# Optimization experiments

Measured on AMD Instinct MI355X. Metric: run time of the kernel, lower is better.

## Reference

```python
import jax, jax.numpy as jnp
import numpy as np

D_MODEL = 512
SCALE = 1.0 / (D_MODEL ** 0.5)  # module scales by 1/sqrt(d_model), not d_head
NEG = -1000000000.0

def setup_inputs() -> dict:
    key = jax.random.key(0)
    kq, kk, kv, kl = jax.random.split(key, 4)
    B, H, S, Dh = 4, 8, 2048, 64
    Q = jax.random.normal(kq, (B, H, S, Dh), dtype=jnp.float32)
    K = jax.random.normal(kk, (B, H, S, Dh), dtype=jnp.float32)
    V = jax.random.normal(kv, (B, H, S, Dh), dtype=jnp.float32)
    src_batch_lens = jax.random.randint(kl, (B,), 1, S + 1, dtype=jnp.int32)
    return {"Q": Q, "K": K, "V": V, "src_batch_lens": src_batch_lens}

def reference(Q, K, V, src_batch_lens):
    # scores: [B, H, Sq, Sk]
    scores = jnp.einsum('bhqd,bhkd->bhqk', Q, K) * SCALE
    Sk = K.shape[2]
    # mask keys at positions >= per-batch length
    key_mask = jnp.arange(Sk)[None, None, None, :] >= src_batch_lens[:, None, None, None]
    scores = jnp.where(key_mask, NEG, scores)
    attn = jax.nn.softmax(scores, axis=-1)
    # dropout is identity in eval/reference (p=0)
    context = jnp.einsum('bhqk,bhkd->bhqd', attn, V)
    return context
```

## Files before the change

kernel.cpp:

```cpp
#include <hip/hip_runtime.h>


#define S_LEN 2048
#define DH 64
#define QK_SCALE ((float)(1.4426950408889634 / 22.627416997969522))
#define NEG_BIG -1.0e30f

typedef __attribute__((ext_vector_type(8))) short bf16x8;
typedef __attribute__((ext_vector_type(4))) float f32x4;

__device__ __forceinline__ short f2bf(float f) {
    __bf16 h = (__bf16)f;
    return __builtin_bit_cast(short, h);
}

#define SW(r, e) ((e) ^ (((r) & 7) << 3))

__global__ __launch_bounds__(256, 2)
void attn_fwd(const float* __restrict__ Qg, const float* __restrict__ Kg,
              const float* __restrict__ Vg, const int* __restrict__ lens,
              float* __restrict__ Og)
{
    __shared__ short Klds[2][64][64];
    __shared__ short Vt[2][64][64];
    __shared__ short Plds[4][16][64];

    const int tid  = threadIdx.x;
    const int wave = tid >> 6;
    const int lane = tid & 63;
    const int lr   = lane & 15;
    const int lg   = lane >> 4;

    const int bh = blockIdx.y;
    const int L  = lens[bh >> 3];
    const int q0 = blockIdx.x * 64 + wave * 16;
    const size_t base = (size_t)bh * S_LEN * DH;

    bf16x8 qf[2];
    {
        const float* qrow = Qg + base + (size_t)(q0 + lr) * DH + 8 * lg;
        #pragma unroll
        for (int ks = 0; ks < 2; ++ks) {
            float4 a = *(const float4*)(qrow + 32 * ks);
            float4 b = *(const float4*)(qrow + 32 * ks + 4);
            bf16x8 f;
            f[0] = f2bf(a.x * QK_SCALE); f[1] = f2bf(a.y * QK_SCALE);
            f[2] = f2bf(a.z * QK_SCALE); f[3] = f2bf(a.w * QK_SCALE);
            f[4] = f2bf(b.x * QK_SCALE); f[5] = f2bf(b.y * QK_SCALE);
            f[6] = f2bf(b.z * QK_SCALE); f[7] = f2bf(b.w * QK_SCALE);
            qf[ks] = f;
        }
    }

    f32x4 Of[4];
    #pragma unroll
    for (int n = 0; n < 4; ++n) Of[n] = (f32x4){0.f, 0.f, 0.f, 0.f};
    f32x4 Dsum = (f32x4){0.f, 0.f, 0.f, 0.f};
    bf16x8 ones;
    #pragma unroll
    for (int j = 0; j < 8; ++j) ones[j] = (short)0x3F80;

    const int ntiles = (L + 63) >> 6;
    const int krow = tid >> 4;
    const int kc4  = tid & 15;

    float4 kreg[4];
    float  vreg[16];

    {
        const float4* kt = (const float4*)(Kg + base);
        #pragma unroll
        for (int it = 0; it < 4; ++it) kreg[it] = kt[(krow + 16 * it) * 16 + kc4];
        const float* vt = Vg + base;
        #pragma unroll
        for (int i = 0; i < 16; ++i) {
            int key = wave * 16 + ((i + (lane >> 3)) & 15);
            vreg[i] = vt[key * DH + lane];
        }
    }
    {
        #pragma unroll
        for (int it = 0; it < 4; ++it) {
            int row = krow + 16 * it;
            short4 s;
            s.x = f2bf(kreg[it].x); s.y = f2bf(kreg[it].y);
            s.z = f2bf(kreg[it].z); s.w = f2bf(kreg[it].w);
            *(short4*)&Klds[0][row][SW(row, kc4 * 4)] = s;
        }
        #pragma unroll
        for (int i = 0; i < 16; ++i) {
            int key = wave * 16 + ((i + (lane >> 3)) & 15);
            Vt[0][lane][SW(lane, key)] = f2bf(vreg[i]);
        }
    }
    __syncthreads();

    for (int t = 0; t < ntiles; ++t) {
        const int cur = t & 1;
        const bool pre = (t + 1 < ntiles);

        if (pre) {
            const float4* kt = (const float4*)(Kg + base + (size_t)(t + 1) * 64 * DH);
            #pragma unroll
            for (int it = 0; it < 4; ++it) kreg[it] = kt[(krow + 16 * it) * 16 + kc4];
            const float* vt = Vg + base + (size_t)(t + 1) * 64 * DH;
            #pragma unroll
            for (int i = 0; i < 16; ++i) {
                int key = wave * 16 + ((i + (lane >> 3)) & 15);
                vreg[i] = vt[key * DH + lane];
            }
        }

        f32x4 Sv[4];
        #pragma unroll
        for (int n = 0; n < 4; ++n) Sv[n] = (f32x4){0.f, 0.f, 0.f, 0.f};
        #pragma unroll
        for (int ks = 0; ks < 2; ++ks) {
            #pragma unroll
            for (int n = 0; n < 4; ++n) {
                bf16x8 kf = *(const bf16x8*)&Klds[cur][16 * n + lr][SW(16 * n + lr, 8 * lg + 32 * ks)];
                Sv[n] = __builtin_amdgcn_mfma_f32_16x16x32_bf16(qf[ks], kf, Sv[n], 0, 0, 0);
            }
        }

        const int kb = t * 64;
        if (kb + 64 > L) {
            #pragma unroll
            for (int n = 0; n < 4; ++n)
                if (kb + 16 * n + lr >= L) {
                    Sv[n][0] = NEG_BIG; Sv[n][1] = NEG_BIG;
                    Sv[n][2] = NEG_BIG; Sv[n][3] = NEG_BIG;
                }
        }

        #pragma unroll
        for (int r = 0; r < 4; ++r) {
            int q = 4 * lg + r;
            #pragma unroll
            for (int n = 0; n < 4; ++n)
                Plds[wave][q][SW(q, 16 * n + lr)] = f2bf(exp2f(Sv[n][r]));
        }

        #pragma unroll
        for (int ks = 0; ks < 2; ++ks) {
            bf16x8 pf = *(const bf16x8*)&Plds[wave][lr][SW(lr, 8 * lg + 32 * ks)];
            Dsum = __builtin_amdgcn_mfma_f32_16x16x32_bf16(pf, ones, Dsum, 0, 0, 0);
            #pragma unroll
            for (int n = 0; n < 4; ++n) {
                bf16x8 vf = *(const bf16x8*)&Vt[cur][16 * n + lr][SW(16 * n + lr, 8 * lg + 32 * ks)];
                Of[n] = __builtin_amdgcn_mfma_f32_16x16x32_bf16(pf, vf, Of[n], 0, 0, 0);
            }
        }

        if (pre) {
            const int b = cur ^ 1;
            #pragma unroll
            for (int it = 0; it < 4; ++it) {
                int row = krow + 16 * it;
                short4 s;
                s.x = f2bf(kreg[it].x); s.y = f2bf(kreg[it].y);
                s.z = f2bf(kreg[it].z); s.w = f2bf(kreg[it].w);
                *(short4*)&Klds[b][row][SW(row, kc4 * 4)] = s;
            }
            #pragma unroll
            for (int i = 0; i < 16; ++i) {
                int key = wave * 16 + ((i + (lane >> 3)) & 15);
                Vt[b][lane][SW(lane, key)] = f2bf(vreg[i]);
            }
        }
        __syncthreads();
    }

    float inv[4];
    #pragma unroll
    for (int r = 0; r < 4; ++r) inv[r] = 1.f / Dsum[r];
    float* orow = Og + base + (size_t)q0 * DH;
    #pragma unroll
    for (int r = 0; r < 4; ++r) {
        int q = 4 * lg + r;
        #pragma unroll
        for (int n = 0; n < 4; ++n)
            orow[(size_t)q * DH + 16 * n + lr] = Of[n][r] * inv[r];
    }
}

extern "C" void kernel_launch(void* const* d_in, const int* in_sizes, int n_in,
                              void* d_out, int out_size, void* d_ws, size_t ws_size,
                              hipStream_t stream) {
    const float* Q = (const float*)d_in[0];
    const float* K = (const float*)d_in[1];
    const float* V = (const float*)d_in[2];
    const int* lens = (const int*)d_in[3];
    float* O = (float*)d_out;
    dim3 grid(S_LEN / 64, 4 * 8);
    attn_fwd<<<grid, 256, 0, stream>>>(Q, K, V, lens, O);
}
```

Baseline: 136.7 us.

## Split key dimension across blocks with workspace partials and a reduce kernel

Adds a grid z-dimension that splits each head's key range into NS chunks. Blocks whose chunk starts past the batch length exit early. Each remaining block writes unnormalised fp16 partial outputs and fp32 denominators to workspace, and a second kernel sums the partials and normalises. It also interleaves the blockIdx.y to batch/head mapping so that short and long batches are mixed across the grid. The aim is to fix load imbalance from varying sequence lengths and make more blocks available, at the cost of extra workspace traffic, a second launch and fp16 rounding of the partial sums.

```diff
diff --git a/kernel.cpp b/kernel.cpp
--- a/kernel.cpp
+++ b/kernel.cpp
@@ -4,7 +4,6 @@
 #define S_LEN 2048
 #define DH 64
 #define QK_SCALE ((float)(1.4426950408889634 / 22.627416997969522))
-#define NEG_BIG -1.0e30f
 
 typedef __attribute__((ext_vector_type(8))) short bf16x8;
 typedef __attribute__((ext_vector_type(4))) float f32x4;
@@ -13,13 +12,21 @@
     __bf16 h = (__bf16)f;
     return __builtin_bit_cast(short, h);
 }
+__device__ __forceinline__ short f2h(float f) {
+    _Float16 h = (_Float16)f;
+    return __builtin_bit_cast(short, h);
+}
+__device__ __forceinline__ float h2f(short s) {
+    return (float)__builtin_bit_cast(_Float16, s);
+}
 
 #define SW(r, e) ((e) ^ (((r) & 7) << 3))
 
 __global__ __launch_bounds__(256, 2)
 void attn_fwd(const float* __restrict__ Qg, const float* __restrict__ Kg,
               const float* __restrict__ Vg, const int* __restrict__ lens,
-              float* __restrict__ Og)
+              float* __restrict__ Og, short* __restrict__ pW,
+              float* __restrict__ dW, int NS, int CH)
 {
     __shared__ short Klds[2][64][64];
     __shared__ short Vt[2][64][64];
@@ -31,8 +38,13 @@
     const int lr   = lane & 15;
     const int lg   = lane >> 4;
 
-    const int bh = blockIdx.y;
+    const int bh = ((blockIdx.y & 3) << 3) | (blockIdx.y >> 2);
     const int L  = lens[bh >> 3];
+    const int start = blockIdx.z * CH;
+    if (start >= L) return;
+    const int end = min(start + CH, L);
+    const int ntiles = (end - start + 63) >> 6;
+
     const int q0 = blockIdx.x * 64 + wave * 16;
     const size_t base = (size_t)bh * S_LEN * DH;
 
@@ -60,7 +72,6 @@
     #pragma unroll
     for (int j = 0; j < 8; ++j) ones[j] = (short)0x3F80;
 
-    const int ntiles = (L + 63) >> 6;
     const int krow = tid >> 4;
     const int kc4  = tid & 15;
 
@@ -68,10 +79,10 @@
     float  vreg[16];
 
     {
-        const float4* kt = (const float4*)(Kg + base);
+        const float4* kt = (const float4*)(Kg + base + (size_t)start * DH);
         #pragma unroll
         for (int it = 0; it < 4; ++it) kreg[it] = kt[(krow + 16 * it) * 16 + kc4];
-        const float* vt = Vg + base;
+        const float* vt = Vg + base + (size_t)start * DH;
         #pragma unroll
         for (int i = 0; i < 16; ++i) {
             int key = wave * 16 + ((i + (lane >> 3)) & 15);
@@ -97,13 +108,14 @@
 
     for (int t = 0; t < ntiles; ++t) {
         const int cur = t & 1;
+        const int kb = start + t * 64;
         const bool pre = (t + 1 < ntiles);
 
         if (pre) {
-            const float4* kt = (const float4*)(Kg + base + (size_t)(t + 1) * 64 * DH);
+            const float4* kt = (const float4*)(Kg + base + (size_t)(kb + 64) * DH);
             #pragma unroll
             for (int it = 0; it < 4; ++it) kreg[it] = kt[(krow + 16 * it) * 16 + kc4];
-            const float* vt = Vg + base + (size_t)(t + 1) * 64 * DH;
+            const float* vt = Vg + base + (size_t)(kb + 64) * DH;
             #pragma unroll
             for (int i = 0; i < 16; ++i) {
                 int key = wave * 16 + ((i + (lane >> 3)) & 15);
@@ -123,13 +135,12 @@
             }
         }
 
-        const int kb = t * 64;
         if (kb + 64 > L) {
             #pragma unroll
             for (int n = 0; n < 4; ++n)
                 if (kb + 16 * n + lr >= L) {
-                    Sv[n][0] = NEG_BIG; Sv[n][1] = NEG_BIG;
-                    Sv[n][2] = NEG_BIG; Sv[n][3] = NEG_BIG;
+                    Sv[n][0] = -1e30f; Sv[n][1] = -1e30f;
+                    Sv[n][2] = -1e30f; Sv[n][3] = -1e30f;
                 }
         }
 
@@ -171,17 +182,56 @@
         __syncthreads();
     }
 
-    float inv[4];
-    #pragma unroll
-    for (int r = 0; r < 4; ++r) inv[r] = 1.f / Dsum[r];
-    float* orow = Og + base + (size_t)q0 * DH;
-    #pragma unroll
-    for (int r = 0; r < 4; ++r) {
-        int q = 4 * lg + r;
-        #pragma unroll
-        for (int n = 0; n < 4; ++n)
-            orow[(size_t)q * DH + 16 * n + lr] = Of[n][r] * inv[r];
-    }
+    if (NS == 1) {
+        float inv[4];
+        #pragma unroll
+        for (int r = 0; r < 4; ++r) inv[r] = 1.f / Dsum[r];
+        float* orow = Og + base + (size_t)q0 * DH;
+        #pragma unroll
+        for (int r = 0; r < 4; ++r) {
+            int q = 4 * lg + r;
+            #pragma unroll
+            for (int n = 0; n < 4; ++n)
+                orow[(size_t)q * DH + 16 * n + lr] = Of[n][r] * inv[r];
+        }
+    } else {
+        short* prow = pW + ((size_t)(blockIdx.z * 32 + bh) * S_LEN + q0) * DH;
+        #pragma unroll
+        for (int r = 0; r < 4; ++r) {
+            int q = 4 * lg + r;
+            #pragma unroll
+            for (int n = 0; n < 4; ++n)
+                prow[(size_t)q * DH + 16 * n + lr] = f2h(Of[n][r]);
+        }
+        if (lr == 0) {
+            #pragma unroll
+            for (int r = 0; r < 4; ++r)
+                dW[(size_t)(blockIdx.z * 32 + bh) * S_LEN + q0 + 4 * lg + r] = Dsum[r];
+        }
+    }
+}
+
+__global__ __launch_bounds__(256)
+void attn_reduce(const int* __restrict__ lens, const short* __restrict__ pW,
+                 const float* __restrict__ dW, float* __restrict__ Og,
+                 int NS, int CH)
+{
+    const size_t i = ((size_t)blockIdx.x * 256 + threadIdx.x) * 4;
+    const int bh = (int)(i >> 17);
+    const int q  = (int)((i >> 6) & (S_LEN - 1));
+    const int L  = lens[bh >> 3];
+    const int nact = min(NS, (L + CH - 1) / CH);
+
+    float ax = 0.f, ay = 0.f, az = 0.f, aw = 0.f, den = 0.f;
+    for (int s = 0; s < nact; ++s) {
+        const size_t sb = (size_t)(s * 32 + bh);
+        short4 h = *(const short4*)(pW + sb * (S_LEN * DH) + (i & (S_LEN * DH - 1)));
+        ax += h2f(h.x); ay += h2f(h.y); az += h2f(h.z); aw += h2f(h.w);
+        den += dW[sb * S_LEN + q];
+    }
+    const float inv = 1.f / den;
+    float4 o; o.x = ax * inv; o.y = ay * inv; o.z = az * inv; o.w = aw * inv;
+    *(float4*)(Og + i) = o;
 }
 
 extern "C" void kernel_launch(void* const* d_in, const int* in_sizes, int n_in,
@@ -192,6 +242,20 @@
     const float* V = (const float*)d_in[2];
     const int* lens = (const int*)d_in[3];
     float* O = (float*)d_out;
-    dim3 grid(S_LEN / 64, 4 * 8);
-    attn_fwd<<<grid, 256, 0, stream>>>(Q, K, V, lens, O);
-}
+
+    const size_t outN = (size_t)4 * 8 * S_LEN * DH;
+    auto need = [&](int ns) {
+        return (size_t)ns * (outN * 2 + (size_t)32 * S_LEN * 4);
+    };
+    int NS = (ws_size >= need(4)) ? 4 : (ws_size >= need(2)) ? 2 : 1;
+    const int CH = S_LEN / NS;
+
+    short* pW = (short*)d_ws;
+    float* dW = (float*)((char*)d_ws + (size_t)NS * outN * 2);
+
+    dim3 grid1(S_LEN / 64, 4 * 8, NS);
+    attn_fwd<<<grid1, 256, 0, stream>>>(Q, K, V, lens, O, pW, dW, NS, CH);
+    if (NS > 1) {
+        attn_reduce<<<(unsigned)(outN / 1024), 256, 0, stream>>>(lens, pW, dW, O, NS, CH);
+    }
+}
```

Result: slower. 147.7 us (+8.1%).

## Vectorize LDS stores for K, V and P tiles, and interleave batch-head block order

Applied to the files above, without the earlier changes.

K tiles are now staged as 8-wide bf16 LDS stores per thread. Each thread writes V transposed as two 16-byte vectors instead of 16 scalar shorts. The QK MFMA operands are swapped so each lane holds 4 consecutive keys of one query row, which lets P be written to LDS as short4 vectors and changes the mask indexing to match. The blockIdx.y to batch-head mapping is permuted so that neighbouring blocks come from different batches, which spreads the variable sequence lengths across the GPU. The aim is fewer LDS write instructions and less bank traffic, plus better load balance; the new V store pattern may bring bank conflicts and changes the global load coalescing for V.

```diff
diff --git a/kernel.cpp b/kernel.cpp
--- a/kernel.cpp
+++ b/kernel.cpp
@@ -4,7 +4,6 @@
 #define S_LEN 2048
 #define DH 64
 #define QK_SCALE ((float)(1.4426950408889634 / 22.627416997969522))
-#define NEG_BIG -1.0e30f
 
 typedef __attribute__((ext_vector_type(8))) short bf16x8;
 typedef __attribute__((ext_vector_type(4))) float f32x4;
@@ -31,7 +30,7 @@
     const int lr   = lane & 15;
     const int lg   = lane >> 4;
 
-    const int bh = blockIdx.y;
+    const int bh = ((blockIdx.y & 3) << 3) | (blockIdx.y >> 2);
     const int L  = lens[bh >> 3];
     const int q0 = blockIdx.x * 64 + wave * 16;
     const size_t base = (size_t)bh * S_LEN * DH;
@@ -61,54 +60,60 @@
     for (int j = 0; j < 8; ++j) ones[j] = (short)0x3F80;
 
     const int ntiles = (L + 63) >> 6;
-    const int krow = tid >> 4;
-    const int kc4  = tid & 15;
+
+    const int krow = tid >> 3;
+    const int kc8  = (tid & 7) * 8;
 
     float4 kreg[4];
     float  vreg[16];
 
     {
-        const float4* kt = (const float4*)(Kg + base);
-        #pragma unroll
-        for (int it = 0; it < 4; ++it) kreg[it] = kt[(krow + 16 * it) * 16 + kc4];
+        const float* kt = Kg + base;
+        #pragma unroll
+        for (int p = 0; p < 2; ++p) {
+            kreg[2 * p]     = *(const float4*)(kt + (krow + 32 * p) * DH + kc8);
+            kreg[2 * p + 1] = *(const float4*)(kt + (krow + 32 * p) * DH + kc8 + 4);
+        }
         const float* vt = Vg + base;
         #pragma unroll
-        for (int i = 0; i < 16; ++i) {
-            int key = wave * 16 + ((i + (lane >> 3)) & 15);
-            vreg[i] = vt[key * DH + lane];
-        }
+        for (int i = 0; i < 16; ++i)
+            vreg[i] = vt[(wave * 16 + i) * DH + lane];
     }
     {
         #pragma unroll
-        for (int it = 0; it < 4; ++it) {
-            int row = krow + 16 * it;
-            short4 s;
-            s.x = f2bf(kreg[it].x); s.y = f2bf(kreg[it].y);
-            s.z = f2bf(kreg[it].z); s.w = f2bf(kreg[it].w);
-            *(short4*)&Klds[0][row][SW(row, kc4 * 4)] = s;
-        }
-        #pragma unroll
-        for (int i = 0; i < 16; ++i) {
-            int key = wave * 16 + ((i + (lane >> 3)) & 15);
-            Vt[0][lane][SW(lane, key)] = f2bf(vreg[i]);
-        }
+        for (int p = 0; p < 2; ++p) {
+            int row = krow + 32 * p;
+            bf16x8 s;
+            s[0] = f2bf(kreg[2*p].x); s[1] = f2bf(kreg[2*p].y);
+            s[2] = f2bf(kreg[2*p].z); s[3] = f2bf(kreg[2*p].w);
+            s[4] = f2bf(kreg[2*p+1].x); s[5] = f2bf(kreg[2*p+1].y);
+            s[6] = f2bf(kreg[2*p+1].z); s[7] = f2bf(kreg[2*p+1].w);
+            *(bf16x8*)&Klds[0][row][SW(row, kc8)] = s;
+        }
+        bf16x8 a, b;
+        #pragma unroll
+        for (int i = 0; i < 8; ++i) { a[i] = f2bf(vreg[i]); b[i] = f2bf(vreg[8 + i]); }
+        *(bf16x8*)&Vt[0][lane][SW(lane, wave * 16)]     = a;
+        *(bf16x8*)&Vt[0][lane][SW(lane, wave * 16 + 8)] = b;
     }
     __syncthreads();
 
     for (int t = 0; t < ntiles; ++t) {
         const int cur = t & 1;
+        const int kb = t * 64;
         const bool pre = (t + 1 < ntiles);
 
         if (pre) {
-            const float4* kt = (const float4*)(Kg + base + (size_t)(t + 1) * 64 * DH);
-            #pragma unroll
-            for (int it = 0; it < 4; ++it) kreg[it] = kt[(krow + 16 * it) * 16 + kc4];
-            const float* vt = Vg + base + (size_t)(t + 1) * 64 * DH;
-            #pragma unroll
-            for (int i = 0; i < 16; ++i) {
-                int key = wave * 16 + ((i + (lane >> 3)) & 15);
-                vreg[i] = vt[key * DH + lane];
-            }
+            const float* kt = Kg + base + (size_t)(kb + 64) * DH;
+            #pragma unroll
+            for (int p = 0; p < 2; ++p) {
+                kreg[2 * p]     = *(const float4*)(kt + (krow + 32 * p) * DH + kc8);
+                kreg[2 * p + 1] = *(const float4*)(kt + (krow + 32 * p) * DH + kc8 + 4);
+            }
+            const float* vt = Vg + base + (size_t)(kb + 64) * DH;
+            #pragma unroll
+            for (int i = 0; i < 16; ++i)
+                vreg[i] = vt[(wave * 16 + i) * DH + lane];
         }
 
         f32x4 Sv[4];
@@ -119,26 +124,28 @@
             #pragma unroll
             for (int n = 0; n < 4; ++n) {
                 bf16x8 kf = *(const bf16x8*)&Klds[cur][16 * n + lr][SW(16 * n + lr, 8 * lg + 32 * ks)];
-                Sv[n] = __builtin_amdgcn_mfma_f32_16x16x32_bf16(qf[ks], kf, Sv[n], 0, 0, 0);
-            }
-        }
-
-        const int kb = t * 64;
+                Sv[n] = __builtin_amdgcn_mfma_f32_16x16x32_bf16(kf, qf[ks], Sv[n], 0, 0, 0);
+            }
+        }
+
         if (kb + 64 > L) {
             #pragma unroll
-            for (int n = 0; n < 4; ++n)
-                if (kb + 16 * n + lr >= L) {
-                    Sv[n][0] = NEG_BIG; Sv[n][1] = NEG_BIG;
-                    Sv[n][2] = NEG_BIG; Sv[n][3] = NEG_BIG;
-                }
-        }
-
-        #pragma unroll
-        for (int r = 0; r < 4; ++r) {
-            int q = 4 * lg + r;
-            #pragma unroll
-            for (int n = 0; n < 4; ++n)
-                Plds[wave][q][SW(q, 16 * n + lr)] = f2bf(exp2f(Sv[n][r]));
+            for (int n = 0; n < 4; ++n) {
+                const int kbase = kb + 16 * n + 4 * lg;
+                #pragma unroll
+                for (int r = 0; r < 4; ++r)
+                    if (kbase + r >= L) Sv[n][r] = -1e30f;
+            }
+        }
+
+        #pragma unroll
+        for (int n = 0; n < 4; ++n) {
+            short4 pq;
+            pq.x = f2bf(exp2f(Sv[n][0]));
+            pq.y = f2bf(exp2f(Sv[n][1]));
+            pq.z = f2bf(exp2f(Sv[n][2]));
+            pq.w = f2bf(exp2f(Sv[n][3]));
+            *(short4*)&Plds[wave][lr][SW(lr, 16 * n + 4 * lg)] = pq;
         }
 
         #pragma unroll
@@ -155,18 +162,20 @@
         if (pre) {
             const int b = cur ^ 1;
             #pragma unroll
-            for (int it = 0; it < 4; ++it) {
-                int row = krow + 16 * it;
-                short4 s;
-                s.x = f2bf(kreg[it].x); s.y = f2bf(kreg[it].y);
-                s.z = f2bf(kreg[it].z); s.w = f2bf(kreg[it].w);
-                *(short4*)&Klds[b][row][SW(row, kc4 * 4)] = s;
-            }
-            #pragma unroll
-            for (int i = 0; i < 16; ++i) {
-                int key = wave * 16 + ((i + (lane >> 3)) & 15);
-                Vt[b][lane][SW(lane, key)] = f2bf(vreg[i]);
-            }
+            for (int p = 0; p < 2; ++p) {
+                int row = krow + 32 * p;
+                bf16x8 s;
+                s[0] = f2bf(kreg[2*p].x); s[1] = f2bf(kreg[2*p].y);
+                s[2] = f2bf(kreg[2*p].z); s[3] = f2bf(kreg[2*p].w);
+                s[4] = f2bf(kreg[2*p+1].x); s[5] = f2bf(kreg[2*p+1].y);
+                s[6] = f2bf(kreg[2*p+1].z); s[7] = f2bf(kreg[2*p+1].w);
+                *(bf16x8*)&Klds[b][row][SW(row, kc8)] = s;
+            }
+            bf16x8 a, bb;
+            #pragma unroll
+            for (int i = 0; i < 8; ++i) { a[i] = f2bf(vreg[i]); bb[i] = f2bf(vreg[8 + i]); }
+            *(bf16x8*)&Vt[b][lane][SW(lane, wave * 16)]     = a;
+            *(bf16x8*)&Vt[b][lane][SW(lane, wave * 16 + 8)] = bb;
         }
         __syncthreads();
     }
```

Measured after the change: 139.1 us. Within noise of the previous version (+1.7%).
